# Kernel tuning notes

Measured on AMD Instinct MI355X. Metric: run time of the kernel, lower is better.

## Reference

```python
import jax, jax.numpy as jnp
import numpy as np

DIM = 2048
NUM_HEADS = 16
NUM_KV_HEADS = 4
HEAD_DIM = DIM // NUM_HEADS
KV_DIM = NUM_KV_HEADS * HEAD_DIM
ROPE_BASE = 10000.0
QK_GAIN_INIT = 1.0
BSZ, SEQ = 4, 2048


def rms_norm(x):
    eps = jnp.finfo(x.dtype).eps
    return x * jax.lax.rsqrt(jnp.mean(x * x, axis=-1, keepdims=True) + eps)


def rope_cos_sin(seqlen, head_dim, base, dtype):
    inv_freq = base ** (-jnp.arange(0, head_dim, 2, dtype=jnp.float32) / head_dim)
    t = jnp.arange(seqlen, dtype=jnp.float32)
    freqs = t[:, None] * inv_freq[None, :]  # [S, hd/2]
    return jnp.cos(freqs).astype(dtype), jnp.sin(freqs).astype(dtype)


def apply_rotary(x, cos, sin):
    # x: [B, H, S, hd]; cos/sin: [S, hd/2]
    x1, x2 = jnp.split(x, 2, axis=-1)
    c = cos[None, None, :, :]
    s = sin[None, None, :, :]
    return jnp.concatenate([x1 * c + x2 * s, -x1 * s + x2 * c], axis=-1)


def setup_inputs() -> dict:
    key = jax.random.key(0)
    ks = jax.random.split(key, 6)
    std = 0.02
    return {
        "x": jax.random.normal(ks[0], (BSZ, SEQ, DIM), dtype=jnp.float32),
        "Wq": jax.random.normal(ks[1], (DIM, DIM), dtype=jnp.float32) * std,
        "Wk": jax.random.normal(ks[2], (KV_DIM, DIM), dtype=jnp.float32) * std,
        "Wv": jax.random.normal(ks[3], (KV_DIM, DIM), dtype=jnp.float32) * std,
        "Wo": jax.random.normal(ks[4], (DIM, DIM), dtype=jnp.float32) * std,
        "q_gain": jnp.full((NUM_HEADS,), QK_GAIN_INIT, dtype=jnp.float32),
    }


def reference(x, Wq, Wk, Wv, Wo, q_gain):
    bsz, seqlen, dim = x.shape
    # QKV projections (F.linear: x @ W.T)
    q = (x @ Wq.T).reshape(bsz, seqlen, NUM_HEADS, HEAD_DIM).transpose(0, 2, 1, 3)
    k = (x @ Wk.T).reshape(bsz, seqlen, NUM_KV_HEADS, HEAD_DIM).transpose(0, 2, 1, 3)
    v = (x @ Wv.T).reshape(bsz, seqlen, NUM_KV_HEADS, HEAD_DIM).transpose(0, 2, 1, 3)
    # QK RMSNorm
    q = rms_norm(q)
    k = rms_norm(k)
    # RoPE
    cos, sin = rope_cos_sin(seqlen, HEAD_DIM, ROPE_BASE, q.dtype)
    q = apply_rotary(q, cos, sin)
    k = apply_rotary(k, cos, sin)
    # per-head gain
    q = q * q_gain.astype(q.dtype)[None, :, None, None]
    # GQA: repeat kv heads
    rep = NUM_HEADS // NUM_KV_HEADS
    k = jnp.repeat(k, rep, axis=1)
    v = jnp.repeat(v, rep, axis=1)
    # causal SDPA
    scale = 1.0 / jnp.sqrt(jnp.asarray(HEAD_DIM, dtype=q.dtype))
    scores = jnp.einsum("bhsd,bhtd->bhst", q, k) * scale
    causal = jnp.tril(jnp.ones((seqlen, seqlen), dtype=bool))
    scores = jnp.where(causal[None, None], scores, jnp.asarray(-jnp.inf, scores.dtype))
    attn = jax.nn.softmax(scores, axis=-1)
    y = jnp.einsum("bhst,bhtd->bhsd", attn, v)
    y = y.transpose(0, 2, 1, 3).reshape(bsz, seqlen, dim)
    return y @ Wo.T
```

## Files before the change

kernel.cpp:

```cpp
#include <hip/hip_runtime.h>
#include <hip/hip_bf16.h>

typedef __hip_bfloat16 bf16;
typedef short s16x8 __attribute__((ext_vector_type(8)));
typedef float f32x4 __attribute__((ext_vector_type(4)));

#define DIM 2048
#define NHEADS 16
#define NKVH 4
#define HD 128
#define KVDIM 512
#define BSZ 4
#define SEQ 2048
#define MROWS (BSZ*SEQ)
#define NQKV (DIM+2*KVDIM)

__device__ __forceinline__ void gld_lds16(const bf16* g, short* l) {
  __builtin_amdgcn_global_load_lds((__attribute__((address_space(1))) void*)(void*)g,
                                   (__attribute__((address_space(3))) void*)l, 16, 0, 0);
}

__global__ __launch_bounds__(256) void cast_all(
    const float* __restrict__ x,  const float* __restrict__ Wq,
    const float* __restrict__ Wk, const float* __restrict__ Wv,
    const float* __restrict__ Wo, bf16* __restrict__ xbf,
    bf16* __restrict__ Wqkv, bf16* __restrict__ Wob) {
  const int i = blockIdx.x*256 + threadIdx.x;
  const float* src; bf16* dst; int j, o;
  if (i < 2097152)      { src = x;  dst = xbf;  j = i;           o = i; }
  else if (i < 2621440) { src = Wq; dst = Wqkv; j = i - 2097152; o = i - 2097152; }
  else if (i < 2752512) { src = Wk; dst = Wqkv; j = i - 2621440; o = i - 2097152; }
  else if (i < 2883584) { src = Wv; dst = Wqkv; j = i - 2752512; o = i - 2097152; }
  else                  { src = Wo; dst = Wob;  j = i - 2883584; o = i - 2883584; }
  const float4* s4 = (const float4*)src;
  float4 a = s4[2*j];
  float4 b = s4[2*j+1];
  union { bf16 h[8]; uint4 u; } pk;
  pk.h[0] = __float2bfloat16(a.x); pk.h[1] = __float2bfloat16(a.y);
  pk.h[2] = __float2bfloat16(a.z); pk.h[3] = __float2bfloat16(a.w);
  pk.h[4] = __float2bfloat16(b.x); pk.h[5] = __float2bfloat16(b.y);
  pk.h[6] = __float2bfloat16(b.z); pk.h[7] = __float2bfloat16(b.w);
  ((uint4*)dst)[o] = pk.u;
}


template<int MQ>
__device__ __forceinline__ void lda(s16x8 (&af)[4][2], const short* pa, int rds) {
#pragma unroll
  for (int fr = 0; fr < 4; fr++)
#pragma unroll
    for (int ks = 0; ks < 2; ks++)
      af[fr][ks] = *(const s16x8*)(pa + ((MQ*4 + fr)*2 + ks)*512 + rds);
}
template<int NQ>
__device__ __forceinline__ void ldb(s16x8 (&bfv)[2][2], const short* pb, int bsub, int rds) {
#pragma unroll
  for (int fc = 0; fc < 2; fc++)
#pragma unroll
    for (int ks = 0; ks < 2; ks++)
      bfv[fc][ks] = *(const s16x8*)(pb + (bsub + (NQ*2 + fc)*2 + ks)*512 + rds);
}
template<int MQ, int NQ>
__device__ __forceinline__ void mmq(f32x4 (&acc)[8][4], const s16x8 (&af)[4][2],
                                    const s16x8 (&bfv)[2][2]) {
#pragma unroll
  for (int fr = 0; fr < 4; fr++)
#pragma unroll
    for (int fc = 0; fc < 2; fc++)
#pragma unroll
      for (int ks = 0; ks < 2; ks++)
        acc[MQ*4+fr][NQ*2+fc] = __builtin_amdgcn_mfma_f32_16x16x32_bf16(
            af[fr][ks], bfv[fc][ks], acc[MQ*4+fr][NQ*2+fc], 0, 0, 0);
}

#define WV6 asm volatile("s_waitcnt vmcnt(6)" ::: "memory")
#define WV0 asm volatile("s_waitcnt vmcnt(0)" ::: "memory")
#define WVN ((void)0)
#define GBAR __builtin_amdgcn_s_barrier()
#define WLK asm volatile("s_waitcnt lgkmcnt(0)" ::: "memory")
#define PRI1 __builtin_amdgcn_s_setprio(1)
#define PRI0 __builtin_amdgcn_s_setprio(0)

#define KT(B_, T_, S1_, S2_, WVX) do {                                          \
    const short* pa = pAr[B_];                                                  \
    const short* pb = pBr[B_];                                                  \
    s16x8 af[4][2], b0f[2][2], b1f[2][2];                                       \
                                                        \
    lda<0>(af, pa, rds); ldb<0>(b0f, pb, bsub, rds);                            \
    if (S1_) {                                                                  \
      gld_lds16(Ab +      (long)((T_)+1)*64 + eA1, &L[1-(B_)][0][4096+wid512]); \
      gld_lds16(Ab + h1 + (long)((T_)+1)*64 + eA1, &L[1-(B_)][1][4096+wid512]); \
    }                                                                           \
    GBAR; WLK; PRI1; mmq<0,0>(acc, af, b0f); PRI0; GBAR;                        \
                                                        \
    ldb<1>(b1f, pb, bsub, rds);                                                 \
    if (S2_) {                                                                  \
      gld_lds16(Ab +      (long)((T_)+2)*64 + eA0, &L[B_][0][wid512]);          \
      gld_lds16(Ab + h1 + (long)((T_)+2)*64 + eA0, &L[B_][1][wid512]);          \
    }                                                                           \
    GBAR; WLK; PRI1; mmq<0,1>(acc, af, b1f); PRI0; GBAR;                        \
                                                        \
    lda<1>(af, pa, rds);                                                        \
    if (S2_) {                                                                  \
      gld_lds16(Bb + (long)((T_)+2)*64 + eA0, &L[B_][2][wid512]);               \
      gld_lds16(Bb + (long)((T_)+2)*64 + eA1, &L[B_][2][4096+wid512]);          \
    }                                                                           \
    GBAR; WLK; PRI1; mmq<1,0>(acc, af, b0f); PRI0; GBAR;                        \
                                                        \
    if (S2_) {                                                                  \
      gld_lds16(Bb + h1 + (long)((T_)+2)*64 + eA0, &L[B_][3][wid512]);          \
      gld_lds16(Bb + h1 + (long)((T_)+2)*64 + eA1, &L[B_][3][4096+wid512]);     \
    }                                                                           \
    WVX;                                                                        \
    GBAR; PRI1; mmq<1,1>(acc, af, b1f); PRI0; GBAR;                             \
  } while (0)

template<int EPI>
__global__ __launch_bounds__(512, 2) void gemm8(
    const bf16* __restrict__ A, const bf16* __restrict__ Bm,
    float* __restrict__ Cf, bf16* __restrict__ Qo, bf16* __restrict__ Ko,
    bf16* __restrict__ Vo, int N, int K) {
  __shared__ short L[2][4][8192] __attribute__((aligned(16)));
  const int tid = threadIdx.x;
  const int lane = tid & 63, wid = tid >> 6;
  const int quad = lane >> 4, l15 = lane & 15;
  const int wm = wid >> 2, wn = wid & 3;

  const int gx  = gridDim.x;
  const int lin = blockIdx.y * gx + blockIdx.x;
  const int cpx = (gx * gridDim.y) >> 3;
  const int swz = (lin & 7) * cpx + (lin >> 3);
  const int m0 = (swz / gx) * 256, n0 = (swz % gx) * 256;

  const int rds = l15*32 + ((quad*8) ^ ((l15 & 8) << 1));
  const int bsub = (wn & 1) * 8;

  const int colx = ((lane & 3) * 8) ^ ((lane >> 5) << 4);
  const int gc   = ((wid & 1) << 5) + colx;
  const int gr0  = ((wid >> 1) << 4) + (lane >> 2);
  const long eA0 = (long)gr0 * K + gc;
  const long eA1 = eA0 + 64L * K;
  const int wid512 = wid * 512;
  const bf16* Ab = A  + (long)m0 * K;
  const bf16* Bb = Bm + (long)n0 * K;
  const long h1 = 128L * K;

  const short* pAr[2] = { &L[0][wm][0], &L[1][wm][0] };
  const short* pBr[2] = { &L[0][2 + (wn >> 1)][0], &L[1][2 + (wn >> 1)][0] };

  f32x4 acc[8][4] = {};

  gld_lds16(Ab + eA0,           &L[0][0][wid512]);
  gld_lds16(Ab + eA1,           &L[0][0][4096 + wid512]);
  gld_lds16(Ab + h1 + eA0,      &L[0][1][wid512]);
  gld_lds16(Ab + h1 + eA1,      &L[0][1][4096 + wid512]);
  gld_lds16(Bb + eA0,           &L[0][2][wid512]);
  gld_lds16(Bb + eA1,           &L[0][2][4096 + wid512]);
  gld_lds16(Bb + h1 + eA0,      &L[0][3][wid512]);
  gld_lds16(Bb + h1 + eA1,      &L[0][3][4096 + wid512]);
  gld_lds16(Ab + 64 + eA0,      &L[1][0][wid512]);
  gld_lds16(Ab + h1 + 64 + eA0, &L[1][1][wid512]);
  gld_lds16(Bb + 64 + eA0,      &L[1][2][wid512]);
  gld_lds16(Bb + 64 + eA1,      &L[1][2][4096 + wid512]);
  gld_lds16(Bb + h1 + 64 + eA0, &L[1][3][wid512]);
  gld_lds16(Bb + h1 + 64 + eA1, &L[1][3][4096 + wid512]);
  WV6;
  GBAR;

  for (int t = 0; t < 30; t += 2) {
    KT(0, t,   1, 1, WV6);
    KT(1, t+1, 1, 1, WV6);
  }
  KT(0, 30, 1, 0, WV0);
  KT(1, 31, 0, 0, WVN);

  const int colg0 = n0 + wn*64;
  const int bb = (m0 + wm*128) >> 11;
  const int sb = (m0 + wm*128) & (SEQ-1);
  if (EPI == 0) {
#pragma unroll
    for (int mi = 0; mi < 8; mi++)
#pragma unroll
      for (int nj = 0; nj < 4; nj++) {
        const int col = colg0 + nj*16 + l15;
#pragma unroll
        for (int r = 0; r < 4; r++)
          Cf[(long)(m0 + wm*128 + mi*16 + quad*4 + r)*N + col] = acc[mi][nj][r];
      }
  } else if (colg0 >= DIM + KVDIM) {
    const int cv = colg0 - (DIM + KVDIM);
    const int h  = cv >> 7;
    const int db = cv & 127;
    bf16* vb = Vo + ((long)(bb*NKVH + h)*HD)*SEQ + sb;
#pragma unroll
    for (int mi = 0; mi < 8; mi++)
#pragma unroll
      for (int nj = 0; nj < 4; nj++) {
        const int d = db + nj*16 + l15;
        union { bf16 h4[4]; unsigned long long u; } pk;
        pk.h4[0] = __float2bfloat16(acc[mi][nj][0]);
        pk.h4[1] = __float2bfloat16(acc[mi][nj][1]);
        pk.h4[2] = __float2bfloat16(acc[mi][nj][2]);
        pk.h4[3] = __float2bfloat16(acc[mi][nj][3]);
        *(unsigned long long*)(vb + (long)d*SEQ + mi*16 + quad*4) = pk.u;
      }
  } else {
    short* ew = &L[0][0][0] + wid*8192;
#pragma unroll
    for (int mi = 0; mi < 8; mi++)
#pragma unroll
      for (int nj = 0; nj < 4; nj++)
#pragma unroll
        for (int r = 0; r < 4; r++) {
          bf16 hv = __float2bfloat16(acc[mi][nj][r]);
          ew[(mi*16 + quad*4 + r)*64 + nj*16 + l15] = *(short*)&hv;
        }
    asm volatile("" ::: "memory");
    bf16* gb;
    if (colg0 < DIM) gb = Qo + (long)(bb*NHEADS + (colg0 >> 7))*SEQ*HD;
    else             gb = Ko + (long)(bb*NKVH + ((colg0 - DIM) >> 7))*SEQ*HD;
    const int db = colg0 & 127;
    const int rr = lane >> 3, c8 = (lane & 7)*8;
#pragma unroll
    for (int it = 0; it < 16; it++) {
      const int row = it*8 + rr;
      uint4 v = *(const uint4*)&ew[row*64 + c8];
      *(uint4*)(gb + (long)(sb + row)*HD + db + c8) = v;
    }
  }
}

__global__ __launch_bounds__(256) void norm_rope(bf16* __restrict__ Qb,
                                                 bf16* __restrict__ Kb,
                                                 const float* __restrict__ gain) {
  const int lane = threadIdx.x & 63, wid = threadIdx.x >> 6;
  const long rid = (long)blockIdx.x*4 + wid;
  const long QR = (long)BSZ*NHEADS*SEQ;
  bf16* ptr; float g; int s;
  if (rid < QR) {
    ptr = Qb + rid*HD;
    s = (int)(rid & (SEQ-1));
    const int h = (int)((rid >> 11) & 15);
    g = gain[h] * 0.08838834764831845f;
  } else {
    const long r2 = rid - QR;
    ptr = Kb + r2*HD;
    s = (int)(r2 & (SEQ-1));
    g = 1.0f;
  }
  float x1 = __bfloat162float(ptr[lane]);
  float x2 = __bfloat162float(ptr[lane+64]);
  float ss = x1*x1 + x2*x2;
#pragma unroll
  for (int off = 1; off < 64; off <<= 1) ss += __shfl_xor(ss, off);
  const float rn = rsqrtf(ss*(1.0f/128.0f) + 1.1920928955078125e-07f);
  const float inv_freq = exp2f((float)lane * -0.20762050593046014f);
  float sn, cs;
  sincosf((float)s * inv_freq, &sn, &cs);
  const float q1 = x1*rn, q2 = x2*rn;
  ptr[lane]    = __float2bfloat16((q1*cs + q2*sn)*g);
  ptr[lane+64] = __float2bfloat16((q2*cs - q1*sn)*g);
}

__global__ __launch_bounds__(256, 2) void attn(
    const bf16* __restrict__ Qb, const bf16* __restrict__ Kb,
    const bf16* __restrict__ Vtg, bf16* __restrict__ Yb) {
  __shared__ short Kt[64*136]  __attribute__((aligned(16)));
  __shared__ short Vt[128*72]  __attribute__((aligned(16)));
  __shared__ short Pt[4*2304]  __attribute__((aligned(16)));

  const int tid = threadIdx.x;
  const int lane = tid & 63, wid = tid >> 6;
  const int quad = lane >> 4, l15 = lane & 15;
  const int xb = blockIdx.x;
  const int bh = blockIdx.y;
  const int b = bh >> 4, h = bh & 15, kvh = h >> 2;

  const bf16* kbase = Kb  + (long)(b*NKVH + kvh)*SEQ*HD;
  const bf16* vbase = Vtg + (long)(b*NKVH + kvh)*HD*SEQ;
  short* pw0 = Pt + wid*2304;
  short* pw1 = pw0 + 1152;
  const int krow = tid >> 4, kc = (tid & 15)*8;
  const int vrow = tid >> 3, vc = (tid & 7)*8;

  for (int phase = 0; phase < 2; phase++) {
    const int qt = phase ? xb : (15 - xb);
    const int q0 = qt*128 + wid*16 + l15;
    const int q1 = q0 + 64;
    const bf16* qr0 = Qb + ((long)(b*NHEADS + h)*SEQ + q0)*HD + quad*8;
    s16x8 qa0[4], qa1[4];
#pragma unroll
    for (int st = 0; st < 4; st++) {
      qa0[st] = *(const s16x8*)(qr0 + st*32);
      qa1[st] = *(const s16x8*)(qr0 + 64*HD + st*32);
    }

    f32x4 o0[8] = {}, o1[8] = {};
    float li0 = 0.0f, li1 = 0.0f;
    const int ktiles = 2*qt + 2;

    for (int kt = 0; kt < ktiles; kt++) {
      __syncthreads();
#pragma unroll
      for (int i = 0; i < 4; i++) {
        uint4 kv = *(const uint4*)(kbase + (long)(kt*64 + i*16 + krow)*HD + kc);
        *(uint4*)&Kt[(i*16 + krow)*136 + kc] = kv;
      }
#pragma unroll
      for (int i = 0; i < 4; i++) {
        uint4 vv = *(const uint4*)(vbase + (long)(i*32 + vrow)*SEQ + kt*64 + vc);
        *(uint4*)&Vt[(i*32 + vrow)*72 + vc] = vv;
      }
      __syncthreads();

      f32x4 s0[4] = {}, s1[4] = {};
#pragma unroll
      for (int nt = 0; nt < 4; nt++) {
        s16x8 kf[4];
#pragma unroll
        for (int st = 0; st < 4; st++)
          kf[st] = *(const s16x8*)&Kt[(nt*16 + l15)*136 + st*32 + quad*8];
#pragma unroll
        for (int st = 0; st < 4; st++) {
          s0[nt] = __builtin_amdgcn_mfma_f32_16x16x32_bf16(kf[st], qa0[st], s0[nt], 0, 0, 0);
          s1[nt] = __builtin_amdgcn_mfma_f32_16x16x32_bf16(kf[st], qa1[st], s1[nt], 0, 0, 0);
        }
      }

      const bool d0 = (kt >= 2*qt);
      const bool d1 = (kt >  2*qt);
      const int tb = kt*64 + quad*4;
      union { bf16 h[16]; unsigned long long u[4]; } p0, p1;
      float rs0 = 0.0f, rs1 = 0.0f;
#pragma unroll
      for (int nt = 0; nt < 4; nt++) {
#pragma unroll
        for (int r = 0; r < 4; r++) {
          const int t = tb + nt*16 + r;
          float v0 = s0[nt][r], v1 = s1[nt][r];
          if (d0 && (t > q0)) v0 = -1e30f;
          if (d1 && (t > q1)) v1 = -1e30f;
          const float e0 = __expf(v0 - 12.0f);
          const float e1 = __expf(v1 - 12.0f);
          rs0 += e0; rs1 += e1;
          p0.h[nt*4+r] = __float2bfloat16(e0);
          p1.h[nt*4+r] = __float2bfloat16(e1);
        }
      }
      li0 += rs0; li1 += rs1;
#pragma unroll
      for (int nt = 0; nt < 4; nt++) {
        *(unsigned long long*)&pw0[l15*72 + nt*16 + quad*4] = p0.u[nt];
        *(unsigned long long*)&pw1[l15*72 + nt*16 + quad*4] = p1.u[nt];
      }

#pragma unroll
      for (int st = 0; st < 2; st++) {
        s16x8 pf0 = *(const s16x8*)&pw0[l15*72 + st*32 + quad*8];
        s16x8 pf1 = *(const s16x8*)&pw1[l15*72 + st*32 + quad*8];
#pragma unroll
        for (int dt = 0; dt < 8; dt++) {
          s16x8 vf = *(const s16x8*)&Vt[(dt*16 + l15)*72 + st*32 + quad*8];
          o0[dt] = __builtin_amdgcn_mfma_f32_16x16x32_bf16(vf, pf0, o0[dt], 0, 0, 0);
          o1[dt] = __builtin_amdgcn_mfma_f32_16x16x32_bf16(vf, pf1, o1[dt], 0, 0, 0);
        }
      }
    }

    li0 += __shfl_xor(li0, 16); li0 += __shfl_xor(li0, 32);
    li1 += __shfl_xor(li1, 16); li1 += __shfl_xor(li1, 32);
    const float inv0 = 1.0f / li0, inv1 = 1.0f / li1;

    short* ep = pw0;
#pragma unroll
    for (int g = 0; g < 2; g++) {
      const float inv = g ? inv1 : inv0;
      const f32x4* o = g ? o1 : o0;
      const int qg = g ? q1 : q0;
#pragma unroll
      for (int dt = 0; dt < 8; dt++) {
        union { bf16 h[4]; unsigned long long u; } pk;
        pk.h[0] = __float2bfloat16(o[dt][0]*inv);
        pk.h[1] = __float2bfloat16(o[dt][1]*inv);
        pk.h[2] = __float2bfloat16(o[dt][2]*inv);
        pk.h[3] = __float2bfloat16(o[dt][3]*inv);
        *(unsigned long long*)&ep[l15*136 + dt*16 + quad*4] = pk.u;
      }
      bf16* yb = Yb + ((long)(b*SEQ + qg - l15))*DIM + h*HD;
#pragma unroll
      for (int p = 0; p < 4; p++) {
        const int c = quad + 4*p;
        uint4 yv = *(const uint4*)&ep[l15*136 + c*8];
        *(uint4*)&yb[(long)l15*DIM + c*8] = yv;
      }
    }
  }
}

extern "C" void kernel_launch(void* const* d_in, const int* in_sizes, int n_in,
                              void* d_out, int out_size, void* d_ws, size_t ws_size,
                              hipStream_t stream) {
  (void)in_sizes; (void)n_in; (void)out_size; (void)ws_size;
  const float* x   = (const float*)d_in[0];
  const float* Wq  = (const float*)d_in[1];
  const float* Wk  = (const float*)d_in[2];
  const float* Wv  = (const float*)d_in[3];
  const float* Wo  = (const float*)d_in[4];
  const float* qg  = (const float*)d_in[5];

  char* ws = (char*)d_ws;
  bf16* xbf  = (bf16*)(ws);
  bf16* Wqkv = (bf16*)(ws + 33554432);
  bf16* Wob  = (bf16*)(ws + 46137344);
  bf16* Qb   = (bf16*)(ws + 54525952);
  bf16* Kb   = (bf16*)(ws + 88080384);
  bf16* Vb   = (bf16*)(ws + 96468992);
  bf16* Yb   = (bf16*)(ws + 104857600);

  cast_all<<<13312, 256, 0, stream>>>(x, Wq, Wk, Wv, Wo, xbf, Wqkv, Wob);

  gemm8<1><<<dim3(NQKV/256, MROWS/256), 512, 0, stream>>>(
      xbf, Wqkv, nullptr, Qb, Kb, Vb, NQKV, DIM);

  norm_rope<<<40960, 256, 0, stream>>>(Qb, Kb, qg);

  attn<<<dim3(8, BSZ*NHEADS), 256, 0, stream>>>(Qb, Kb, Vb, Yb);

  gemm8<0><<<dim3(DIM/256, MROWS/256), 512, 0, stream>>>(
      Yb, Wob, (float*)d_out, nullptr, nullptr, nullptr, DIM, DIM);
}
```

Measured before the change: 439.4 us.

## Prefetch K/V tiles in registers, swizzle attention grid, stage GEMM output via LDS

The attention kernel now loads the next K/V tile into registers while it computes on the current one, so global-load latency overlaps with MFMA work. It also remaps the block index so blocks sharing a KV head are scheduled near each other, and wraps the MFMA loops in priority macros (PRI1/PRI0). The fp32 output GEMM epilogue now stages accumulators through LDS so each row is written with coalesced float4 stores instead of scattered scalar stores. The cost is extra registers per thread and possible LDS reuse hazards in the epilogue.

Measured after the change: 443.4 us. About the same (+0.9%).

```diff
diff --git a/kernel.cpp b/kernel.cpp
--- a/kernel.cpp
+++ b/kernel.cpp
@@ -178,15 +178,27 @@
   const int bb = (m0 + wm*128) >> 11;
   const int sb = (m0 + wm*128) & (SEQ-1);
   if (EPI == 0) {
-#pragma unroll
-    for (int mi = 0; mi < 8; mi++)
-#pragma unroll
-      for (int nj = 0; nj < 4; nj++) {
-        const int col = colg0 + nj*16 + l15;
-#pragma unroll
-        for (int r = 0; r < 4; r++)
-          Cf[(long)(m0 + wm*128 + mi*16 + quad*4 + r)*N + col] = acc[mi][nj][r];
-      }
+    float* ew = (float*)(&L[0][0][0]) + wid*4096;
+    const int rowb = m0 + wm*128;
+    const int rr = lane >> 3, c4 = (lane & 7)*4;
+#pragma unroll
+    for (int half = 0; half < 2; half++) {
+#pragma unroll
+      for (int mi = 0; mi < 8; mi++)
+#pragma unroll
+        for (int nj2 = 0; nj2 < 2; nj2++)
+#pragma unroll
+          for (int r = 0; r < 4; r++)
+            ew[(mi*16 + quad*4 + r)*32 + nj2*16 + l15] = acc[mi][half*2 + nj2][r];
+      asm volatile("" ::: "memory");
+#pragma unroll
+      for (int it = 0; it < 16; it++) {
+        const int row = it*8 + rr;
+        float4 v = *(const float4*)&ew[row*32 + c4];
+        *(float4*)(Cf + (long)(rowb + row)*N + colg0 + half*32 + c4) = v;
+      }
+      asm volatile("" ::: "memory");
+    }
   } else if (colg0 >= DIM + KVDIM) {
     const int cv = colg0 - (DIM + KVDIM);
     const int h  = cv >> 7;
@@ -272,8 +284,10 @@
   const int tid = threadIdx.x;
   const int lane = tid & 63, wid = tid >> 6;
   const int quad = lane >> 4, l15 = lane & 15;
-  const int xb = blockIdx.x;
-  const int bh = blockIdx.y;
+  const int lin = blockIdx.y*8 + blockIdx.x;
+  const int swz = (lin & 7)*64 + (lin >> 3);
+  const int xb = swz & 7;
+  const int bh = swz >> 3;
   const int b = bh >> 4, h = bh & 15, kvh = h >> 2;
 
   const bf16* kbase = Kb  + (long)(b*NKVH + kvh)*SEQ*HD;
@@ -283,6 +297,19 @@
   const int krow = tid >> 4, kc = (tid & 15)*8;
   const int vrow = tid >> 3, vc = (tid & 7)*8;
 
+#define LOADK(KT_) do {                                                        \
+    kr0 = *(const uint4*)(kbase + (long)((KT_)*64 +  0 + krow)*HD + kc);       \
+    kr1 = *(const uint4*)(kbase + (long)((KT_)*64 + 16 + krow)*HD + kc);       \
+    kr2 = *(const uint4*)(kbase + (long)((KT_)*64 + 32 + krow)*HD + kc);       \
+    kr3 = *(const uint4*)(kbase + (long)((KT_)*64 + 48 + krow)*HD + kc);       \
+  } while (0)
+#define LOADV(KT_) do {                                                        \
+    vr0 = *(const uint4*)(vbase + (long)(  0 + vrow)*SEQ + (KT_)*64 + vc);     \
+    vr1 = *(const uint4*)(vbase + (long)( 32 + vrow)*SEQ + (KT_)*64 + vc);     \
+    vr2 = *(const uint4*)(vbase + (long)( 64 + vrow)*SEQ + (KT_)*64 + vc);     \
+    vr3 = *(const uint4*)(vbase + (long)( 96 + vrow)*SEQ + (KT_)*64 + vc);     \
+  } while (0)
+
   for (int phase = 0; phase < 2; phase++) {
     const int qt = phase ? xb : (15 - xb);
     const int q0 = qt*128 + wid*16 + l15;
@@ -299,19 +326,21 @@
     float li0 = 0.0f, li1 = 0.0f;
     const int ktiles = 2*qt + 2;
 
+    uint4 kr0, kr1, kr2, kr3, vr0, vr1, vr2, vr3;
+    LOADK(0); LOADV(0);
+
     for (int kt = 0; kt < ktiles; kt++) {
       __syncthreads();
-#pragma unroll
-      for (int i = 0; i < 4; i++) {
-        uint4 kv = *(const uint4*)(kbase + (long)(kt*64 + i*16 + krow)*HD + kc);
-        *(uint4*)&Kt[(i*16 + krow)*136 + kc] = kv;
-      }
-#pragma unroll
-      for (int i = 0; i < 4; i++) {
-        uint4 vv = *(const uint4*)(vbase + (long)(i*32 + vrow)*SEQ + kt*64 + vc);
-        *(uint4*)&Vt[(i*32 + vrow)*72 + vc] = vv;
-      }
+      *(uint4*)&Kt[( 0 + krow)*136 + kc] = kr0;
+      *(uint4*)&Kt[(16 + krow)*136 + kc] = kr1;
+      *(uint4*)&Kt[(32 + krow)*136 + kc] = kr2;
+      *(uint4*)&Kt[(48 + krow)*136 + kc] = kr3;
+      *(uint4*)&Vt[(  0 + vrow)*72 + vc] = vr0;
+      *(uint4*)&Vt[( 32 + vrow)*72 + vc] = vr1;
+      *(uint4*)&Vt[( 64 + vrow)*72 + vc] = vr2;
+      *(uint4*)&Vt[( 96 + vrow)*72 + vc] = vr3;
       __syncthreads();
+      if (kt + 1 < ktiles) { LOADK(kt+1); LOADV(kt+1); }
 
       f32x4 s0[4] = {}, s1[4] = {};
 #pragma unroll
@@ -320,11 +349,13 @@
 #pragma unroll
         for (int st = 0; st < 4; st++)
           kf[st] = *(const s16x8*)&Kt[(nt*16 + l15)*136 + st*32 + quad*8];
+        PRI1;
 #pragma unroll
         for (int st = 0; st < 4; st++) {
           s0[nt] = __builtin_amdgcn_mfma_f32_16x16x32_bf16(kf[st], qa0[st], s0[nt], 0, 0, 0);
           s1[nt] = __builtin_amdgcn_mfma_f32_16x16x32_bf16(kf[st], qa1[st], s1[nt], 0, 0, 0);
         }
+        PRI0;
       }
 
       const bool d0 = (kt >= 2*qt);
@@ -358,12 +389,14 @@
       for (int st = 0; st < 2; st++) {
         s16x8 pf0 = *(const s16x8*)&pw0[l15*72 + st*32 + quad*8];
         s16x8 pf1 = *(const s16x8*)&pw1[l15*72 + st*32 + quad*8];
+        PRI1;
 #pragma unroll
         for (int dt = 0; dt < 8; dt++) {
           s16x8 vf = *(const s16x8*)&Vt[(dt*16 + l15)*72 + st*32 + quad*8];
           o0[dt] = __builtin_amdgcn_mfma_f32_16x16x32_bf16(vf, pf0, o0[dt], 0, 0, 0);
           o1[dt] = __builtin_amdgcn_mfma_f32_16x16x32_bf16(vf, pf1, o1[dt], 0, 0, 0);
         }
+        PRI0;
       }
     }
 
@@ -395,6 +428,8 @@
       }
     }
   }
+#undef LOADK
+#undef LOADV
 }
 
 extern "C" void kernel_launch(void* const* d_in, const int* in_sizes, int n_in,
```
